# Optimization experiments

Measured on AMD Instinct MI355X. Metric: run time of the kernel, lower is better.

## Reference

```python
import jax, jax.numpy as jnp
import numpy as np

N = 100000   # nodes
E = 1600000  # edges (before self-loops)
D = 128      # input_dim
H = 128      # hidden_dim


def setup_inputs() -> dict:
    key = jax.random.key(0)
    ks = jax.random.split(key, 10)
    def lin_w(k, fan_in, fan_out):
        return jax.random.normal(k, (fan_in, fan_out), jnp.float32) / np.float32(np.sqrt(fan_in))
    x = jax.random.normal(ks[0], (N, D), jnp.float32)
    edge_index = jax.random.randint(ks[1], (2, E), 0, N)
    return {
        "x": x,
        "edge_index": edge_index,
        "W0": lin_w(ks[2], D, H), "b0": jnp.zeros((H,), jnp.float32),
        "W1": lin_w(ks[3], H, H), "b1": jnp.zeros((H,), jnp.float32),
        "W2": lin_w(ks[4], H, H), "b2": jnp.zeros((H,), jnp.float32),
        "Wr": lin_w(ks[5], D, H), "br": jnp.zeros((H,), jnp.float32),
    }


def _gcn_norm(edge_index, n):
    # add self-loops, then symmetric normalization D^{-1/2} (A+I) D^{-1/2}
    loop = jnp.arange(n, dtype=edge_index.dtype)
    src = jnp.concatenate([edge_index[0], loop])
    dst = jnp.concatenate([edge_index[1], loop])
    deg = jax.ops.segment_sum(jnp.ones_like(src, dtype=jnp.float32), dst, num_segments=n)
    dinv = jnp.where(deg > 0, jax.lax.rsqrt(deg), 0.0)
    norm = dinv[src] * dinv[dst]  # [E+N]
    return src, dst, norm


def _gcn_layer(x, W, b, src, dst, norm, n):
    h = x @ W                      # [n, H] dense GEMM
    msg = h[src] * norm[:, None]   # gather + scale  [E+N, H]
    out = jax.ops.segment_sum(msg, dst, num_segments=n)  # scatter-add
    return out + b


def reference(x, edge_index, W0, b0, W1, b1, W2, b2, Wr, br):
    n = x.shape[0]
    src, dst, norm = _gcn_norm(edge_index, n)
    residual = x @ Wr + br
    # layer 0: GCN -> relu -> (dropout=identity, eval) -> +residual
    h = jax.nn.relu(_gcn_layer(x, W0, b0, src, dst, norm, n)) + residual
    # layer 1
    h = jax.nn.relu(_gcn_layer(h, W1, b1, src, dst, norm, n))
    # layer 2
    h = jax.nn.relu(_gcn_layer(h, W2, b2, src, dst, norm, n))
    return h
```

## Files before the change

### kernel.cpp

```cpp
#include <hip/hip_runtime.h>
#include <hip/hip_bf16.h>
#include <cstdint>


#define WS_ALIGN(x) (((x) + 255) & ~(size_t)255)

typedef __bf16 bf16x8 __attribute__((ext_vector_type(8)));
typedef float  floatx4 __attribute__((ext_vector_type(4)));

static __device__ __forceinline__ float bf_lo(unsigned u) {
  return __builtin_bit_cast(float, u << 16);
}
static __device__ __forceinline__ float bf_hi(unsigned u) {
  return __builtin_bit_cast(float, u & 0xffff0000u);
}
static __device__ __forceinline__ unsigned short f2bs(float f) {
  unsigned u = __builtin_bit_cast(unsigned, f);
  return (unsigned short)((u + 0x7fffu + ((u >> 16) & 1u)) >> 16);
}
static __device__ __forceinline__ unsigned pack2(float a, float b) {
  return (unsigned)f2bs(a) | ((unsigned)f2bs(b) << 16);
}

__global__ void k_prep(const float* __restrict__ x, unsigned* __restrict__ xb, int n4,
                       int* __restrict__ cnt, int n,
                       const float* __restrict__ W0, const float* __restrict__ W1,
                       const float* __restrict__ W2, const float* __restrict__ Wr,
                       unsigned short* __restrict__ Wt,
                       unsigned short* __restrict__ A, int* __restrict__ ovfn,
                       int zb, int xbn) {
  int b = blockIdx.x;
  if (b < zb) {
    int i = b * 256 + threadIdx.x;
    if (i < n) cnt[i] = 0;
  } else if (b < zb + xbn) {
    int i = (b - zb) * 256 + threadIdx.x;
    if (i < n4) {
      float4 v = ((const float4*)x)[i];
      uint2 o;
      o.x = pack2(v.x, v.y);
      o.y = pack2(v.z, v.w);
      ((uint2*)xb)[i] = o;
    }
  } else {
    int wb = b - zb - xbn;
    if (wb < 256) {
      int mat = wb >> 6, blk = wb & 63;
      const float* W = mat == 0 ? W0 : mat == 1 ? W1 : mat == 2 ? W2 : Wr;
      unsigned short* T = Wt + (size_t)mat * 16384;
      int i = blk * 256 + threadIdx.x;
      int k = i >> 7, nn = i & 127;
      T[nn * 128 + k] = f2bs(W[i]);
    } else {
      if (threadIdx.x < 16) {
        uint4 z; z.x = 0; z.y = 0; z.z = 0; z.w = 0;
        ((uint4*)(A + (size_t)n * 128))[threadIdx.x] = z;
      }
      if (threadIdx.x == 16) *ovfn = 0;
    }
  }
}

__global__ __launch_bounds__(256, 2) void k_gemm_mfma(
    const unsigned short* __restrict__ Xb,
    const unsigned short* __restrict__ Wt,
    const float* __restrict__ bias,
    const float* __restrict__ dv,
    unsigned short* __restrict__ Y,
    int n) {
  __shared__ unsigned short sWt[128 * 128];
  {
    const uint4* s4 = (const uint4*)Wt;
    uint4* d4 = (uint4*)sWt;
    for (int i = threadIdx.x; i < 2048; i += 256) d4[i] = s4[i];
  }
  __syncthreads();

  const int lane = threadIdx.x & 63;
  const int wave = threadIdx.x >> 6;
  const int l15 = lane & 15;
  const int quad = lane >> 4;
  const int rbase = blockIdx.x * 64 + wave * 16;

  const bf16x8* sW8 = (const bf16x8*)sWt;
  bf16x8 b[8][4];
#pragma unroll
  for (int ct = 0; ct < 8; ct++)
#pragma unroll
    for (int kc = 0; kc < 4; kc++)
      b[ct][kc] = sW8[(ct * 16 + l15) * 16 + kc * 4 + quad];

  int row = rbase + l15;
  row = row < n ? row : n - 1;
  const bf16x8* X8 = (const bf16x8*)Xb;
  bf16x8 a[4];
#pragma unroll
  for (int kc = 0; kc < 4; kc++)
    a[kc] = X8[(size_t)row * 16 + kc * 4 + quad];

  floatx4 acc[8];
#pragma unroll
  for (int ct = 0; ct < 8; ct++) acc[ct] = (floatx4){0.f, 0.f, 0.f, 0.f};

#pragma unroll
  for (int kc = 0; kc < 4; kc++)
#pragma unroll
    for (int ct = 0; ct < 8; ct++)
      acc[ct] = __builtin_amdgcn_mfma_f32_16x16x32_bf16(a[kc], b[ct][kc], acc[ct], 0, 0, 0);

  const int orow = rbase + quad * 4;
  float4 dvv;
  dvv.x = 1.f; dvv.y = 1.f; dvv.z = 1.f; dvv.w = 1.f;
  if (dv) {
    int od = orow < n ? orow : 0;
    dvv = *(const float4*)(dv + od);
  }
#pragma unroll
  for (int ct = 0; ct < 8; ct++) {
    const int c = ct * 16 + l15;
    const float bv = bias ? bias[c] : 0.f;
#pragma unroll
    for (int r4 = 0; r4 < 4; r4++) {
      int r = orow + r4;
      float dm = r4 == 0 ? dvv.x : r4 == 1 ? dvv.y : r4 == 2 ? dvv.z : dvv.w;
      if (r < n) Y[(size_t)r * 128 + c] = f2bs(acc[ct][r4] * dm + bv);
    }
  }
}

__global__ void k_fill1p(const int* __restrict__ srcv, const int* __restrict__ dstv,
                         int E, int* __restrict__ cnt, int* __restrict__ epk,
                         int2* __restrict__ ovf, int* __restrict__ ovfn) {
  int e = blockIdx.x * blockDim.x + threadIdx.x;
  if (e < E) {
    int s = srcv[e], d = dstv[e];
    int rank = atomicAdd(&cnt[d], 1);
    if (rank < 32) {
      epk[(size_t)d * 32 + rank] = s;
    } else {
      int o = atomicAdd(ovfn, 1);
      if (o < E) {
        int2 t; t.x = s; t.y = d;
        ovf[o] = t;
      }
    }
  }
}

__global__ void k_aux(const int* __restrict__ cnt, float* __restrict__ dinv,
                      int* __restrict__ epk, int n) {
  int i = blockIdx.x * 256 + threadIdx.x;
  if (i < n) {
    int c = cnt[i];
    dinv[i] = rsqrtf((float)(c + 1));
    int cm = c < 32 ? c : 32;
    int cp = (cm + 7) & ~7;
    for (int k = cm; k < cp; k++) epk[(size_t)i * 32 + k] = n;
  }
}

static __device__ __forceinline__ void add8(uint4 h, float* a) {
  a[0] += bf_lo(h.x); a[1] += bf_hi(h.x);
  a[2] += bf_lo(h.y); a[3] += bf_hi(h.y);
  a[4] += bf_lo(h.z); a[5] += bf_hi(h.z);
  a[6] += bf_lo(h.w); a[7] += bf_hi(h.w);
}

__global__ __launch_bounds__(256, 4) void k_agg(
    const uint4* __restrict__ H,
    const int* __restrict__ cnt,
    const int* __restrict__ epk,
    const float* __restrict__ dinv,
    const float* __restrict__ bias,
    const uint4* __restrict__ resid,
    uint4* __restrict__ outb,
    float4* __restrict__ outf,
    const int2* __restrict__ ovf, const int* __restrict__ ovfn,
    int n, int Ecap) {
  int node = blockIdx.x * 16 + (threadIdx.x >> 4);
  int l = threadIdx.x & 15;
  if (node >= n) return;

  int tot = cnt[node];
  int cm = tot < 32 ? tot : 32;
  int pdeg = (cm + 7) & ~7;

  uint4 hv = H[(size_t)node * 16 + l];
  float a[8];
  a[0] = bf_lo(hv.x); a[1] = bf_hi(hv.x);
  a[2] = bf_lo(hv.y); a[3] = bf_hi(hv.y);
  a[4] = bf_lo(hv.z); a[5] = bf_hi(hv.z);
  a[6] = bf_lo(hv.w); a[7] = bf_hi(hv.w);

  const int4* epk4 = (const int4*)(epk + (size_t)node * 32);
  for (int j = 0; j < pdeg; j += 8) {
    int4 e0 = epk4[j >> 2];
    int4 e1 = epk4[(j >> 2) + 1];
    uint4 h0 = H[(size_t)(unsigned)e0.x * 16 + l];
    uint4 h1 = H[(size_t)(unsigned)e0.y * 16 + l];
    uint4 h2 = H[(size_t)(unsigned)e0.z * 16 + l];
    uint4 h3 = H[(size_t)(unsigned)e0.w * 16 + l];
    uint4 h4 = H[(size_t)(unsigned)e1.x * 16 + l];
    uint4 h5 = H[(size_t)(unsigned)e1.y * 16 + l];
    uint4 h6 = H[(size_t)(unsigned)e1.z * 16 + l];
    uint4 h7 = H[(size_t)(unsigned)e1.w * 16 + l];
    add8(h0, a); add8(h1, a); add8(h2, a); add8(h3, a);
    add8(h4, a); add8(h5, a); add8(h6, a); add8(h7, a);
  }
  if (tot > 32) {
    int no = *ovfn;
    no = no < Ecap ? no : Ecap;
    for (int i = 0; i < no; i++) {
      int2 t = ovf[i];
      if (t.y == node) add8(H[(size_t)(unsigned)t.x * 16 + l], a);
    }
  }

  float dn = dinv[node];
  float4 bl = ((const float4*)bias)[l * 2];
  float4 bh = ((const float4*)bias)[l * 2 + 1];
  a[0] = fmaxf(fmaf(a[0], dn, bl.x), 0.f); a[1] = fmaxf(fmaf(a[1], dn, bl.y), 0.f);
  a[2] = fmaxf(fmaf(a[2], dn, bl.z), 0.f); a[3] = fmaxf(fmaf(a[3], dn, bl.w), 0.f);
  a[4] = fmaxf(fmaf(a[4], dn, bh.x), 0.f); a[5] = fmaxf(fmaf(a[5], dn, bh.y), 0.f);
  a[6] = fmaxf(fmaf(a[6], dn, bh.z), 0.f); a[7] = fmaxf(fmaf(a[7], dn, bh.w), 0.f);
  if (resid) {
    uint4 r = resid[(size_t)node * 16 + l];
    a[0] += bf_lo(r.x); a[1] += bf_hi(r.x);
    a[2] += bf_lo(r.y); a[3] += bf_hi(r.y);
    a[4] += bf_lo(r.z); a[5] += bf_hi(r.z);
    a[6] += bf_lo(r.w); a[7] += bf_hi(r.w);
  }
  if (outb) {
    uint4 o;
    o.x = pack2(a[0], a[1]); o.y = pack2(a[2], a[3]);
    o.z = pack2(a[4], a[5]); o.w = pack2(a[6], a[7]);
    outb[(size_t)node * 16 + l] = o;
  } else {
    float4 o0; o0.x = a[0]; o0.y = a[1]; o0.z = a[2]; o0.w = a[3];
    float4 o1; o1.x = a[4]; o1.y = a[5]; o1.z = a[6]; o1.w = a[7];
    outf[(size_t)node * 32 + l * 2] = o0;
    outf[(size_t)node * 32 + l * 2 + 1] = o1;
  }
}

extern "C" void kernel_launch(void* const* d_in, const int* in_sizes, int n_in,
                              void* d_out, int out_size, void* d_ws, size_t ws_size,
                              hipStream_t stream) {
  const float* x  = (const float*)d_in[0];
  const int* edges = (const int*)d_in[1];
  const float* W0 = (const float*)d_in[2];
  const float* b0 = (const float*)d_in[3];
  const float* W1 = (const float*)d_in[4];
  const float* b1 = (const float*)d_in[5];
  const float* W2 = (const float*)d_in[6];
  const float* b2 = (const float*)d_in[7];
  const float* Wr = (const float*)d_in[8];
  const float* br = (const float*)d_in[9];

  int N = in_sizes[0] / 128;
  int E = in_sizes[1] / 2;
  const int* src = edges;
  const int* dst = edges + E;

  char* ws = (char*)d_ws;
  size_t off = 0;
  auto alloc = [&](size_t bytes) -> void* {
    void* p = ws + off; off = WS_ALIGN(off + bytes); return p;
  };
  int*   cnt  = (int*)  alloc((size_t)N * 4);
  float* dinv = (float*)alloc((size_t)N * 4);
  int*   ovfn = (int*)  alloc(256);
  int2*  ovf  = (int2*) alloc((size_t)E * 8);
  int*   epk  = (int*)  alloc((size_t)N * 32 * 4);
  unsigned short* xb = (unsigned short*)alloc((size_t)N * 128 * 2);
  unsigned short* Wt = (unsigned short*)alloc((size_t)4 * 16384 * 2);
  unsigned short* A  = (unsigned short*)alloc(((size_t)N + 1) * 128 * 2);
  unsigned short* Hb = (unsigned short*)alloc((size_t)N * 128 * 2);
  unsigned short* R  = (unsigned short*)alloc((size_t)N * 128 * 2);
  (void)ws_size; (void)n_in; (void)out_size;

  int n4 = N * 128 / 4;
  int zb = (N + 255) / 256;
  int xbn = (n4 + 255) / 256;
  k_prep<<<zb + xbn + 257, 256, 0, stream>>>(x, (unsigned*)xb, n4, cnt, N,
                                             W0, W1, W2, Wr, Wt, A, ovfn, zb, xbn);

  int gb = (N + 63) / 64;
  int eb = (E + 255) / 256;
  unsigned short* Wt0 = Wt;
  unsigned short* Wt1 = Wt + 16384;
  unsigned short* Wt2 = Wt + 2 * 16384;
  unsigned short* Wtr = Wt + 3 * 16384;
  k_fill1p<<<eb, 256, 0, stream>>>(src, dst, E, cnt, epk, ovf, ovfn);
  k_gemm_mfma<<<gb, 256, 0, stream>>>(xb, Wtr, br, nullptr, R, N);
  k_aux<<<(N + 255) / 256, 256, 0, stream>>>(cnt, dinv, epk, N);

  int ab = (N + 15) / 16;

  k_gemm_mfma<<<gb, 256, 0, stream>>>(xb, Wt0, nullptr, dinv, A, N);
  k_agg<<<ab, 256, 0, stream>>>((const uint4*)A, cnt, epk, dinv, b0,
                                (const uint4*)R, (uint4*)Hb, nullptr, ovf, ovfn, N, E);
  k_gemm_mfma<<<gb, 256, 0, stream>>>(Hb, Wt1, nullptr, dinv, A, N);
  k_agg<<<ab, 256, 0, stream>>>((const uint4*)A, cnt, epk, dinv, b1,
                                nullptr, (uint4*)R, nullptr, ovf, ovfn, N, E);
  k_gemm_mfma<<<gb, 256, 0, stream>>>(R, Wt2, nullptr, dinv, A, N);
  k_agg<<<ab, 256, 0, stream>>>((const uint4*)A, cnt, epk, dinv, b2,
                                nullptr, nullptr, (float4*)d_out, ovf, ovfn, N, E);
}
```

Baseline: 515.0 us.

## Split edge bucketing into count and scatter passes; aggregate two nodes per group

The single-pass fill kernel is split into a counting kernel that records each edge's rank and a separate scatter kernel that writes the neighbour lists. The rank array reuses the A buffer as scratch, and the residual GEMM is launched between the two passes. The aggregation kernel now has each 16-lane group handle two nodes, interleaving their gathers to raise memory-level parallelism, with half as many blocks. The cost is an extra launch and an extra pass over the edge list, plus higher register pressure in the aggregation kernel and wasted dummy gathers when the two nodes have unequal degrees.

```diff
diff --git a/kernel.cpp b/kernel.cpp
--- a/kernel.cpp
+++ b/kernel.cpp
@@ -61,6 +61,44 @@
   }
 }
 
+__global__ void k_cnt(const int* __restrict__ dstv, int E,
+                      int* __restrict__ cnt, int* __restrict__ pos) {
+  int e = blockIdx.x * blockDim.x + threadIdx.x;
+  if (e < E) pos[e] = atomicAdd(&cnt[dstv[e]], 1);
+}
+
+__global__ void k_scat(const int* __restrict__ srcv, const int* __restrict__ dstv,
+                       const int* __restrict__ pos, int E,
+                       int* __restrict__ epk, int2* __restrict__ ovf,
+                       int* __restrict__ ovfn) {
+  int e = blockIdx.x * blockDim.x + threadIdx.x;
+  if (e < E) {
+    int s = srcv[e], d = dstv[e];
+    int r = pos[e];
+    if (r < 32) {
+      epk[(size_t)d * 32 + r] = s;
+    } else {
+      int o = atomicAdd(ovfn, 1);
+      if (o < E) {
+        int2 t; t.x = s; t.y = d;
+        ovf[o] = t;
+      }
+    }
+  }
+}
+
+__global__ void k_aux(const int* __restrict__ cnt, float* __restrict__ dinv,
+                      int* __restrict__ epk, int n) {
+  int i = blockIdx.x * 256 + threadIdx.x;
+  if (i < n) {
+    int c = cnt[i];
+    dinv[i] = rsqrtf((float)(c + 1));
+    int cm = c < 32 ? c : 32;
+    int cp = (cm + 7) & ~7;
+    for (int k = cm; k < cp; k++) epk[(size_t)i * 32 + k] = n;
+  }
+}
+
 __global__ __launch_bounds__(256, 2) void k_gemm_mfma(
     const unsigned short* __restrict__ Xb,
     const unsigned short* __restrict__ Wt,
@@ -128,37 +166,6 @@
   }
 }
 
-__global__ void k_fill1p(const int* __restrict__ srcv, const int* __restrict__ dstv,
-                         int E, int* __restrict__ cnt, int* __restrict__ epk,
-                         int2* __restrict__ ovf, int* __restrict__ ovfn) {
-  int e = blockIdx.x * blockDim.x + threadIdx.x;
-  if (e < E) {
-    int s = srcv[e], d = dstv[e];
-    int rank = atomicAdd(&cnt[d], 1);
-    if (rank < 32) {
-      epk[(size_t)d * 32 + rank] = s;
-    } else {
-      int o = atomicAdd(ovfn, 1);
-      if (o < E) {
-        int2 t; t.x = s; t.y = d;
-        ovf[o] = t;
-      }
-    }
-  }
-}
-
-__global__ void k_aux(const int* __restrict__ cnt, float* __restrict__ dinv,
-                      int* __restrict__ epk, int n) {
-  int i = blockIdx.x * 256 + threadIdx.x;
-  if (i < n) {
-    int c = cnt[i];
-    dinv[i] = rsqrtf((float)(c + 1));
-    int cm = c < 32 ? c : 32;
-    int cp = (cm + 7) & ~7;
-    for (int k = cm; k < cp; k++) epk[(size_t)i * 32 + k] = n;
-  }
-}
-
 static __device__ __forceinline__ void add8(uint4 h, float* a) {
   a[0] += bf_lo(h.x); a[1] += bf_hi(h.x);
   a[2] += bf_lo(h.y); a[3] += bf_hi(h.y);
@@ -177,69 +184,130 @@
     float4* __restrict__ outf,
     const int2* __restrict__ ovf, const int* __restrict__ ovfn,
     int n, int Ecap) {
-  int node = blockIdx.x * 16 + (threadIdx.x >> 4);
+  int grp = blockIdx.x * 16 + (threadIdx.x >> 4);
   int l = threadIdx.x & 15;
-  if (node >= n) return;
-
-  int tot = cnt[node];
-  int cm = tot < 32 ? tot : 32;
-  int pdeg = (cm + 7) & ~7;
-
-  uint4 hv = H[(size_t)node * 16 + l];
-  float a[8];
-  a[0] = bf_lo(hv.x); a[1] = bf_hi(hv.x);
-  a[2] = bf_lo(hv.y); a[3] = bf_hi(hv.y);
-  a[4] = bf_lo(hv.z); a[5] = bf_hi(hv.z);
-  a[6] = bf_lo(hv.w); a[7] = bf_hi(hv.w);
-
-  const int4* epk4 = (const int4*)(epk + (size_t)node * 32);
-  for (int j = 0; j < pdeg; j += 8) {
-    int4 e0 = epk4[j >> 2];
-    int4 e1 = epk4[(j >> 2) + 1];
-    uint4 h0 = H[(size_t)(unsigned)e0.x * 16 + l];
-    uint4 h1 = H[(size_t)(unsigned)e0.y * 16 + l];
-    uint4 h2 = H[(size_t)(unsigned)e0.z * 16 + l];
-    uint4 h3 = H[(size_t)(unsigned)e0.w * 16 + l];
-    uint4 h4 = H[(size_t)(unsigned)e1.x * 16 + l];
-    uint4 h5 = H[(size_t)(unsigned)e1.y * 16 + l];
-    uint4 h6 = H[(size_t)(unsigned)e1.z * 16 + l];
-    uint4 h7 = H[(size_t)(unsigned)e1.w * 16 + l];
-    add8(h0, a); add8(h1, a); add8(h2, a); add8(h3, a);
-    add8(h4, a); add8(h5, a); add8(h6, a); add8(h7, a);
-  }
-  if (tot > 32) {
+  int n0 = grp * 2;
+  int n1 = n0 + 1;
+  if (n0 >= n) return;
+  bool has1 = (n1 < n);
+
+  int t0 = cnt[n0];
+  int t1 = has1 ? cnt[n1] : 0;
+  int c0 = t0 < 32 ? t0 : 32;
+  int c1 = t1 < 32 ? t1 : 32;
+  int p0 = (c0 + 7) & ~7;
+  int p1 = has1 ? ((c1 + 7) & ~7) : 0;
+
+  uint4 hv0 = H[(size_t)n0 * 16 + l];
+  uint4 hv1 = H[(size_t)(has1 ? n1 : n) * 16 + l];
+
+  float a0[8], a1[8];
+  a0[0] = bf_lo(hv0.x); a0[1] = bf_hi(hv0.x);
+  a0[2] = bf_lo(hv0.y); a0[3] = bf_hi(hv0.y);
+  a0[4] = bf_lo(hv0.z); a0[5] = bf_hi(hv0.z);
+  a0[6] = bf_lo(hv0.w); a0[7] = bf_hi(hv0.w);
+  a1[0] = bf_lo(hv1.x); a1[1] = bf_hi(hv1.x);
+  a1[2] = bf_lo(hv1.y); a1[3] = bf_hi(hv1.y);
+  a1[4] = bf_lo(hv1.z); a1[5] = bf_hi(hv1.z);
+  a1[6] = bf_lo(hv1.w); a1[7] = bf_hi(hv1.w);
+
+  const int4* q0 = (const int4*)(epk + (size_t)n0 * 32);
+  const int4* q1 = (const int4*)(epk + (size_t)(has1 ? n1 : n0) * 32);
+  int4 zq; zq.x = n; zq.y = n; zq.z = n; zq.w = n;
+
+  int jm = p0 > p1 ? p0 : p1;
+  for (int j = 0; j < jm; j += 8) {
+    bool d0 = j < p0, d1 = j < p1;
+    int4 e0a = d0 ? q0[j >> 2] : zq;
+    int4 e0b = d0 ? q0[(j >> 2) + 1] : zq;
+    int4 e1a = d1 ? q1[j >> 2] : zq;
+    int4 e1b = d1 ? q1[(j >> 2) + 1] : zq;
+    uint4 h00 = H[(size_t)(unsigned)e0a.x * 16 + l];
+    uint4 h01 = H[(size_t)(unsigned)e0a.y * 16 + l];
+    uint4 h02 = H[(size_t)(unsigned)e0a.z * 16 + l];
+    uint4 h03 = H[(size_t)(unsigned)e0a.w * 16 + l];
+    uint4 h10 = H[(size_t)(unsigned)e1a.x * 16 + l];
+    uint4 h11 = H[(size_t)(unsigned)e1a.y * 16 + l];
+    uint4 h12 = H[(size_t)(unsigned)e1a.z * 16 + l];
+    uint4 h13 = H[(size_t)(unsigned)e1a.w * 16 + l];
+    uint4 h04 = H[(size_t)(unsigned)e0b.x * 16 + l];
+    uint4 h05 = H[(size_t)(unsigned)e0b.y * 16 + l];
+    uint4 h06 = H[(size_t)(unsigned)e0b.z * 16 + l];
+    uint4 h07 = H[(size_t)(unsigned)e0b.w * 16 + l];
+    uint4 h14 = H[(size_t)(unsigned)e1b.x * 16 + l];
+    uint4 h15 = H[(size_t)(unsigned)e1b.y * 16 + l];
+    uint4 h16 = H[(size_t)(unsigned)e1b.z * 16 + l];
+    uint4 h17 = H[(size_t)(unsigned)e1b.w * 16 + l];
+    add8(h00, a0); add8(h10, a1);
+    add8(h01, a0); add8(h11, a1);
+    add8(h02, a0); add8(h12, a1);
+    add8(h03, a0); add8(h13, a1);
+    add8(h04, a0); add8(h14, a1);
+    add8(h05, a0); add8(h15, a1);
+    add8(h06, a0); add8(h16, a1);
+    add8(h07, a0); add8(h17, a1);
+  }
+
+  if (t0 > 32 || t1 > 32) {
     int no = *ovfn;
     no = no < Ecap ? no : Ecap;
     for (int i = 0; i < no; i++) {
       int2 t = ovf[i];
-      if (t.y == node) add8(H[(size_t)(unsigned)t.x * 16 + l], a);
-    }
-  }
-
-  float dn = dinv[node];
+      if (t0 > 32 && t.y == n0) add8(H[(size_t)(unsigned)t.x * 16 + l], a0);
+      if (has1 && t1 > 32 && t.y == n1) add8(H[(size_t)(unsigned)t.x * 16 + l], a1);
+    }
+  }
+
   float4 bl = ((const float4*)bias)[l * 2];
   float4 bh = ((const float4*)bias)[l * 2 + 1];
-  a[0] = fmaxf(fmaf(a[0], dn, bl.x), 0.f); a[1] = fmaxf(fmaf(a[1], dn, bl.y), 0.f);
-  a[2] = fmaxf(fmaf(a[2], dn, bl.z), 0.f); a[3] = fmaxf(fmaf(a[3], dn, bl.w), 0.f);
-  a[4] = fmaxf(fmaf(a[4], dn, bh.x), 0.f); a[5] = fmaxf(fmaf(a[5], dn, bh.y), 0.f);
-  a[6] = fmaxf(fmaf(a[6], dn, bh.z), 0.f); a[7] = fmaxf(fmaf(a[7], dn, bh.w), 0.f);
+  float dn0 = dinv[n0];
+  float dn1 = has1 ? dinv[n1] : 0.f;
+
+  a0[0] = fmaxf(fmaf(a0[0], dn0, bl.x), 0.f); a0[1] = fmaxf(fmaf(a0[1], dn0, bl.y), 0.f);
+  a0[2] = fmaxf(fmaf(a0[2], dn0, bl.z), 0.f); a0[3] = fmaxf(fmaf(a0[3], dn0, bl.w), 0.f);
+  a0[4] = fmaxf(fmaf(a0[4], dn0, bh.x), 0.f); a0[5] = fmaxf(fmaf(a0[5], dn0, bh.y), 0.f);
+  a0[6] = fmaxf(fmaf(a0[6], dn0, bh.z), 0.f); a0[7] = fmaxf(fmaf(a0[7], dn0, bh.w), 0.f);
+  a1[0] = fmaxf(fmaf(a1[0], dn1, bl.x), 0.f); a1[1] = fmaxf(fmaf(a1[1], dn1, bl.y), 0.f);
+  a1[2] = fmaxf(fmaf(a1[2], dn1, bl.z), 0.f); a1[3] = fmaxf(fmaf(a1[3], dn1, bl.w), 0.f);
+  a1[4] = fmaxf(fmaf(a1[4], dn1, bh.x), 0.f); a1[5] = fmaxf(fmaf(a1[5], dn1, bh.y), 0.f);
+  a1[6] = fmaxf(fmaf(a1[6], dn1, bh.z), 0.f); a1[7] = fmaxf(fmaf(a1[7], dn1, bh.w), 0.f);
+
   if (resid) {
-    uint4 r = resid[(size_t)node * 16 + l];
-    a[0] += bf_lo(r.x); a[1] += bf_hi(r.x);
-    a[2] += bf_lo(r.y); a[3] += bf_hi(r.y);
-    a[4] += bf_lo(r.z); a[5] += bf_hi(r.z);
-    a[6] += bf_lo(r.w); a[7] += bf_hi(r.w);
+    uint4 r0 = resid[(size_t)n0 * 16 + l];
+    a0[0] += bf_lo(r0.x); a0[1] += bf_hi(r0.x);
+    a0[2] += bf_lo(r0.y); a0[3] += bf_hi(r0.y);
+    a0[4] += bf_lo(r0.z); a0[5] += bf_hi(r0.z);
+    a0[6] += bf_lo(r0.w); a0[7] += bf_hi(r0.w);
+    if (has1) {
+      uint4 r1 = resid[(size_t)n1 * 16 + l];
+      a1[0] += bf_lo(r1.x); a1[1] += bf_hi(r1.x);
+      a1[2] += bf_lo(r1.y); a1[3] += bf_hi(r1.y);
+      a1[4] += bf_lo(r1.z); a1[5] += bf_hi(r1.z);
+      a1[6] += bf_lo(r1.w); a1[7] += bf_hi(r1.w);
+    }
   }
   if (outb) {
-    uint4 o;
-    o.x = pack2(a[0], a[1]); o.y = pack2(a[2], a[3]);
-    o.z = pack2(a[4], a[5]); o.w = pack2(a[6], a[7]);
-    outb[(size_t)node * 16 + l] = o;
+    uint4 o0;
+    o0.x = pack2(a0[0], a0[1]); o0.y = pack2(a0[2], a0[3]);
+    o0.z = pack2(a0[4], a0[5]); o0.w = pack2(a0[6], a0[7]);
+    outb[(size_t)n0 * 16 + l] = o0;
+    if (has1) {
+      uint4 o1;
+      o1.x = pack2(a1[0], a1[1]); o1.y = pack2(a1[2], a1[3]);
+      o1.z = pack2(a1[4], a1[5]); o1.w = pack2(a1[6], a1[7]);
+      outb[(size_t)n1 * 16 + l] = o1;
+    }
   } else {
-    float4 o0; o0.x = a[0]; o0.y = a[1]; o0.z = a[2]; o0.w = a[3];
-    float4 o1; o1.x = a[4]; o1.y = a[5]; o1.z = a[6]; o1.w = a[7];
-    outf[(size_t)node * 32 + l * 2] = o0;
-    outf[(size_t)node * 32 + l * 2 + 1] = o1;
+    float4 o0a; o0a.x = a0[0]; o0a.y = a0[1]; o0a.z = a0[2]; o0a.w = a0[3];
+    float4 o0b; o0b.x = a0[4]; o0b.y = a0[5]; o0b.z = a0[6]; o0b.w = a0[7];
+    outf[(size_t)n0 * 32 + l * 2] = o0a;
+    outf[(size_t)n0 * 32 + l * 2 + 1] = o0b;
+    if (has1) {
+      float4 o1a; o1a.x = a1[0]; o1a.y = a1[1]; o1a.z = a1[2]; o1a.w = a1[3];
+      float4 o1b; o1b.x = a1[4]; o1b.y = a1[5]; o1b.z = a1[6]; o1b.w = a1[7];
+      outf[(size_t)n1 * 32 + l * 2] = o1a;
+      outf[(size_t)n1 * 32 + l * 2 + 1] = o1b;
+    }
   }
 }
 
@@ -277,6 +345,7 @@
   unsigned short* A  = (unsigned short*)alloc(((size_t)N + 1) * 128 * 2);
   unsigned short* Hb = (unsigned short*)alloc((size_t)N * 128 * 2);
   unsigned short* R  = (unsigned short*)alloc((size_t)N * 128 * 2);
+  int* pos = (int*)A;
   (void)ws_size; (void)n_in; (void)out_size;
 
   int n4 = N * 128 / 4;
@@ -291,11 +360,12 @@
   unsigned short* Wt1 = Wt + 16384;
   unsigned short* Wt2 = Wt + 2 * 16384;
   unsigned short* Wtr = Wt + 3 * 16384;
-  k_fill1p<<<eb, 256, 0, stream>>>(src, dst, E, cnt, epk, ovf, ovfn);
+  k_cnt<<<eb, 256, 0, stream>>>(dst, E, cnt, pos);
   k_gemm_mfma<<<gb, 256, 0, stream>>>(xb, Wtr, br, nullptr, R, N);
+  k_scat<<<eb, 256, 0, stream>>>(src, dst, pos, E, epk, ovf, ovfn);
   k_aux<<<(N + 255) / 256, 256, 0, stream>>>(cnt, dinv, epk, N);
 
-  int ab = (N + 15) / 16;
+  int ab = (N + 31) / 32;
 
   k_gemm_mfma<<<gb, 256, 0, stream>>>(xb, Wt0, nullptr, dinv, A, N);
   k_agg<<<ab, 256, 0, stream>>>((const uint4*)A, cnt, epk, dinv, b0,
```

Result: slower. 729.6 us (+41.7%).
